# Kernel optimization log

Measured on AMD Instinct MI355X. Metric: run time of the kernel, lower is better.

The kernel has to match this reference:

```python
import jax, jax.numpy as jnp
import numpy as np


def conv2d(x, w, b):
    # x: [B,C,H,W], w: [O,I,5,5], VALID, stride 1 (matches torch Conv2d defaults)
    y = jax.lax.conv_general_dilated(x, w, (1, 1), 'VALID',
                                     dimension_numbers=('NCHW', 'OIHW', 'NCHW'))
    return y + b[None, :, None, None]


def maxpool_2x5(x):
    # MaxPool2d(kernel=(2,5), stride=(2,1))
    return jax.lax.reduce_window(x, -jnp.inf, jax.lax.max,
                                 (1, 1, 2, 5), (1, 1, 2, 1), 'VALID')


def gru(x, w_ih, w_hh, b_ih, b_hh):
    # Faithful torch nn.GRU (batch_first=False): x is [L, N, 64]; gate order r,z,n.
    H = w_hh.shape[1]
    h0 = jnp.zeros((x.shape[1], H), x.dtype)

    def step(h, xt):
        gi = xt @ w_ih.T + b_ih
        gh = h @ w_hh.T + b_hh
        i_r, i_z, i_n = jnp.split(gi, 3, axis=-1)
        h_r, h_z, h_n = jnp.split(gh, 3, axis=-1)
        r = jax.nn.sigmoid(i_r + h_r)
        z = jax.nn.sigmoid(i_z + h_z)
        n = jnp.tanh(i_n + r * h_n)
        h_new = (1.0 - z) * n + z * h
        return h_new, h_new

    _, ys = jax.lax.scan(step, h0, x)
    return ys


def branch(x, w1, b1, w2, b2, w3, b3, lw, lb, gwih, gwhh, gbih, gbhh):
    x = x[:, None]                      # [B,1,H,W]
    x = conv2d(x, w1, b1)
    x = conv2d(x, w2, b2)
    x = conv2d(x, w3, b3)
    x = maxpool_2x5(x)                  # [B,64,58,W']
    B = x.shape[0]
    x = x.reshape(B, x.shape[-1], 3712)  # same row-major reshape as torch
    x = x @ lw.T + lb                   # [B,W',64]
    # nn.GRU without batch_first scans over dim 0 (batch!) — replicate exactly
    return gru(x, gwih, gwhh, gbih, gbhh)


def _make_params(key):
    ks = iter(jax.random.split(key, 40))
    def p(shape, scale=0.05):
        return (jax.random.normal(next(ks), shape, jnp.float32) * scale)
    d = {}
    for pre in ('e', 't'):
        d[f'{pre}_w1'] = p((16, 1, 5, 5)); d[f'{pre}_b1'] = p((16,))
        d[f'{pre}_w2'] = p((32, 16, 5, 5)); d[f'{pre}_b2'] = p((32,))
        d[f'{pre}_w3'] = p((64, 32, 5, 5)); d[f'{pre}_b3'] = p((64,))
        d[f'{pre}l_w'] = p((64, 3712), 0.01); d[f'{pre}l_b'] = p((64,))
        d[f'{pre}g_wih'] = p((192, 64)); d[f'{pre}g_whh'] = p((192, 64))
        d[f'{pre}g_bih'] = p((192,)); d[f'{pre}g_bhh'] = p((192,))
    d['a_w'] = p((1, 64)); d['a_b'] = p((1,))
    d['h_w'] = p((128, 64)); d['h_b'] = p((128,))
    d['c_w'] = p((2, 128)); d['c_b'] = p((2,))
    return d


def setup_inputs() -> dict:
    key = jax.random.key(0)
    k1, k2, k3 = jax.random.split(key, 3)
    inp = {
        'evaluation': jax.random.normal(k1, (4, 128, 2048), jnp.float32),
        'template': jax.random.normal(k2, (4, 128, 1040), jnp.float32),
    }
    inp.update(_make_params(k3))
    return inp


def reference(evaluation, template,
              e_w1, e_b1, e_w2, e_b2, e_w3, e_b3, el_w, el_b,
              eg_wih, eg_whh, eg_bih, eg_bhh,
              t_w1, t_b1, t_w2, t_b2, t_w3, t_b3, tl_w, tl_b,
              tg_wih, tg_whh, tg_bih, tg_bhh,
              a_w, a_b, h_w, h_b, c_w, c_b):
    e = branch(evaluation, e_w1, e_b1, e_w2, e_b2, e_w3, e_b3,
               el_w, el_b, eg_wih, eg_whh, eg_bih, eg_bhh)   # [B,Se,64]
    t = branch(template, t_w1, t_b1, t_w2, t_b2, t_w3, t_b3,
               tl_w, tl_b, tg_wih, tg_whh, tg_bih, tg_bhh)   # [B,St,64]
    # bmm(template, eval^T) -> [B,St,Se], softmax over Se
    tt = jax.nn.softmax(jnp.einsum('btd,bed->bte', t, e), axis=-1)
    # bmm(tt^T, template) -> [B,Se,64]
    tt = jnp.einsum('bte,btd->bed', tt, t)
    tt = jnp.abs(tt - e)
    # attention over eval sequence positions
    att = jax.nn.softmax((e @ a_w.T + a_b)[..., 0], axis=-1)  # [B,Se]
    # vectorized form of the original Python double loop
    red = jnp.einsum('bed,be->bd', tt, att)                   # [B,64]
    h = jax.nn.relu(red @ h_w.T + h_b)
    return jax.nn.softmax(h @ c_w.T + c_b, axis=-1)           # [B,2]
```

## Files before the change

### kernel.cpp

```cpp
#include <hip/hip_runtime.h>
#include <cmath>


typedef unsigned short u16;
typedef unsigned int u32;
typedef __attribute__((ext_vector_type(8))) short bf16x8;
typedef __attribute__((ext_vector_type(8))) unsigned short u16x8;
typedef __attribute__((ext_vector_type(16))) float f32x16;

__device__ __forceinline__ u16 f2bf(float f) {
  unsigned int x = __float_as_uint(f);
  return (u16)((x + 0x7fffu + ((x >> 16) & 1u)) >> 16);
}
__device__ __forceinline__ float bf2f(u16 v) {
  return __uint_as_float(((unsigned int)v) << 16);
}

static const size_t OFF_BEFF_E  = 0;
static const size_t OFF_BEFF_T  = 64;
static const size_t OFF_BIAS2_E = 128;
static const size_t OFF_BIAS2_T = 320;
static const size_t OFF_WKX_E   = 512;
static const size_t OFF_WKX_T   = 27136;
static const size_t OFF_W12P_E  = 53760;
static const size_t OFF_W12P_T  = 63008;
static const size_t OFF_B12_E   = 72256;
static const size_t OFF_B12_T   = 72288;
static const size_t OFF_LWBF_E  = 72320;
static const size_t OFF_LWBF_T  = 191104;
static const size_t OFF_ATT     = 309888;
static const size_t OFF_XYBF_E  = 318016;
static const size_t OFF_XYBF_T  = 578112;
static const size_t OFF_TTBF    = 709184;
static const size_t OFF_LIN_E   = 840256;
static const size_t OFF_LIN_T   = 1360448;
static const size_t OFF_PV      = 1622592;
static const size_t OFF_RED     = 2142784;
static const size_t ZERO_F4     = 325696;
static const size_t OFF_POOL_E  = 2143040;
static const size_t OFF_POOL_T  = 17228608;
static const size_t OFF_GI_E    = 2143040;
static const size_t OFF_GI_T    = 3703616;
static const size_t OFF_P       = 4490048;

__global__ __launch_bounds__(320) void prep_kernel(
    const float* __restrict__ w1e, const float* __restrict__ b1e,
    const float* __restrict__ w2e, const float* __restrict__ b2e,
    const float* __restrict__ w1t, const float* __restrict__ b1t,
    const float* __restrict__ w2t, const float* __restrict__ b2t,
    float* __restrict__ w12p_e, float* __restrict__ w12p_t,
    float* __restrict__ b12o_e, float* __restrict__ b12o_t,
    const float* __restrict__ wih_e, const float* __restrict__ bih_e,
    const float* __restrict__ lb_e, float* __restrict__ bias2_e,
    const float* __restrict__ wih_t, const float* __restrict__ bih_t,
    const float* __restrict__ lb_t, float* __restrict__ bias2_t,
    const float* __restrict__ lwe, const float* __restrict__ lwt,
    u16* __restrict__ lwbf_e, u16* __restrict__ lwbf_t,
    float4* __restrict__ zbase) {
  const int bx = blockIdx.x;
  const int tid = threadIdx.x;
  {
    const size_t base = (size_t)bx * 615;
    const float4 z = {0.f, 0.f, 0.f, 0.f};
    for (size_t i = base + tid; i < base + 615 && i < ZERO_F4; i += 320)
      zbase[i] = z;
  }
  if (bx >= 66) {
    if (tid < 256) {
      const int k = bx - 66;
      const int br = k / 232, j = k - br * 232;
      const float* src = br ? lwt : lwe;
      u16* dst = br ? lwbf_t : lwbf_e;
      const int i = (j * 256 + tid) * 4;
      const float4 v = *(const float4*)&src[i];
      dst[i] = f2bf(v.x); dst[i + 1] = f2bf(v.y);
      dst[i + 2] = f2bf(v.z); dst[i + 3] = f2bf(v.w);
    }
    return;
  }
  if (bx >= 64) {
    const int br = bx - 64;
    const float* wih = br ? wih_t : wih_e;
    const float* bih = br ? bih_t : bih_e;
    const float* lb = br ? lb_t : lb_e;
    float* bias2 = br ? bias2_t : bias2_e;
    __shared__ float s_lb[64];
    if (tid < 64) s_lb[tid] = lb[tid];
    __syncthreads();
    if (tid < 192) {
      float acc = bih[tid];
      const float* wr = wih + tid * 64;
      for (int d = 0; d < 64; ++d) acc = fmaf(wr[d], s_lb[d], acc);
      bias2[tid] = acc;
    }
    return;
  }
  const int br = bx >> 5;
  const float* w1 = br ? w1t : w1e;
  const float* b1 = br ? b1t : b1e;
  const float* w2 = br ? w2t : w2e;
  const float* b2 = br ? b2t : b2e;
  float* w12p = br ? w12p_t : w12p_e;
  float* b12o = br ? b12o_t : b12o_e;
  const int c12 = bx & 31;
  __shared__ float s_w1pad[16 * 169];
  __shared__ float s_w2c[400];
  __shared__ float s_b1[16];
  for (int i = tid; i < 2704; i += 320) s_w1pad[i] = 0.f;
  if (tid < 16) s_b1[tid] = b1[tid];
  __syncthreads();
  for (int i = tid; i < 400; i += 320) {
    const int c1 = i / 25, r = (i % 25) / 5, cc = i % 5;
    s_w1pad[c1 * 169 + (r + 4) * 13 + (cc + 4)] = w1[i];
    s_w2c[i] = w2[c12 * 400 + i];
  }
  __syncthreads();
  if (tid < 289) {
    const int py = tid / 17, px = tid % 17;
    float v = 0.f;
    if (py >= 4 && py <= 12 && px >= 4 && px <= 12) {
      const int sy = py - 4, sx = px - 4;
      float accs[2] = {0.f, 0.f};
      for (int c1 = 0; c1 < 16; ++c1) {
        const float* w2p = s_w2c + c1 * 25;
        const float* w1p = s_w1pad + c1 * 169 + (sy + 4) * 13 + (sx + 4);
#pragma unroll
        for (int uy = 0; uy < 5; ++uy)
#pragma unroll
          for (int ux = 0; ux < 5; ++ux)
            accs[uy & 1] = fmaf(w2p[uy * 5 + ux], w1p[-(uy * 13) - ux], accs[uy & 1]);
      }
      v = accs[0] + accs[1];
    }
    w12p[c12 * 289 + tid] = v;
  } else if (tid == 300) {
    float acc = b2[c12];
    for (int c1 = 0; c1 < 16; ++c1) {
      float sw = 0.f;
      for (int u = 0; u < 25; ++u) sw += s_w2c[c1 * 25 + u];
      acc = fmaf(sw, s_b1[c1], acc);
    }
    b12o[c12] = acc;
  }
}

__global__ __launch_bounds__(256) void compose_weff_kernel(
    const float* __restrict__ w3e, const float* __restrict__ b3e,
    const float* __restrict__ w3t, const float* __restrict__ b3t,
    const float* __restrict__ w12p_e, const float* __restrict__ w12p_t,
    const float* __restrict__ b12_e, const float* __restrict__ b12_t,
    u16* __restrict__ wkx_e, u16* __restrict__ wkx_t,
    float* __restrict__ beff_e, float* __restrict__ beff_t) {
  const int br = blockIdx.y;
  const float* w3 = br ? w3t : w3e;
  const float* b3 = br ? b3t : b3e;
  const float* w12p = br ? w12p_t : w12p_e;
  const float* b12 = br ? b12_t : b12_e;
  u16* wkx = br ? wkx_t : wkx_e;
  float* beff = br ? beff_t : beff_e;
  const int o = blockIdx.x;
  __shared__ float s_pad[32 * 289];
  __shared__ float s_w3o[800];
  __shared__ float s_b12[32];
  const int tid = threadIdx.x;
  for (int i = tid; i < 9248; i += 256) s_pad[i] = w12p[i];
  for (int i = tid; i < 800; i += 256) s_w3o[i] = w3[o * 800 + i];
  if (tid < 32) s_b12[tid] = b12[tid];
  __syncthreads();
  if (tid < 169) {
    const int sy = tid / 13, sx = tid % 13;
    float accs[4] = {0.f, 0.f, 0.f, 0.f};
#pragma unroll 4
    for (int c = 0; c < 32; ++c) {
      const float* w3p = s_w3o + c * 25;
      const float* wp = s_pad + c * 289 + (sy + 4) * 17 + (sx + 4);
#pragma unroll
      for (int uy = 0; uy < 5; ++uy)
#pragma unroll
        for (int ux = 0; ux < 5; ++ux)
          accs[c & 3] = fmaf(w3p[uy * 5 + ux], wp[-(uy * 17) - ux], accs[c & 3]);
    }
    const u16 v = f2bf(accs[0] + accs[1] + accs[2] + accs[3]);
#pragma unroll
    for (int p = 0; p < 4; ++p)
      wkx[((p * 13 + sx) * 64 + o) * 16 + sy + p] = v;
  } else if (tid < 169 + 156) {
    const int t = tid - 169, kx = t / 12, q = t % 12;
    const int p = q / 3, idx = q % 3;
    const int slot = (idx < p) ? idx : (p + 13) + (idx - p);
    wkx[((p * 13 + kx) * 64 + o) * 16 + slot] = 0;
  } else if (tid == 330 - 5) {
  }
  if (tid == 255) {
    float acc = b3[o];
    for (int c = 0; c < 32; ++c) {
      float sw = 0.f;
      for (int u = 0; u < 25; ++u) sw += s_w3o[c * 25 + u];
      acc = fmaf(sw, s_b12[c], acc);
    }
    beff[o] = acc;
  }
}

__global__ __launch_bounds__(256, 4) void conv_pool_mfma_kernel(
    const float* __restrict__ xe, const u16* __restrict__ wkx_e,
    const float* __restrict__ beff_e, u16* __restrict__ pooled_e,
    const float* __restrict__ xt, const u16* __restrict__ wkx_t,
    const float* __restrict__ beff_t, u16* __restrict__ pooled_t) {
  const int zz = blockIdx.z;
  const bool ev = zz < 4;
  const int b = ev ? zz : zz - 4;
  const int W = ev ? 2048 : 1040;
  const int T = ev ? 2032 : 1024;
  const int cb = blockIdx.x * 60;
  if (cb >= T) return;
  const float* x = ev ? xe : xt;
  const u16* wkx = ev ? wkx_e : wkx_t;
  const float* beff = ev ? beff_e : beff_t;
  u16* pooled = ev ? pooled_e : pooled_t;

  __shared__ __align__(16) u16 s_x[80 * 24];
  __shared__ __align__(16) u16 s_out[2 * 64 * 66];
  __shared__ __align__(16) u16 s_pool[64 * 62];

  const int tid = threadIdx.x;
  const int lane = tid & 63, wave = tid >> 6;
  const int by = blockIdx.y;
  const int rsel = wave & 1, cm = (wave >> 1) * 32;
  const int l31 = lane & 31, g8 = (lane >> 5) * 8;
  const int r0 = 4 * by;

  {
    const float* xb = x + ((size_t)b * 128 + r0) * W;
    for (int i = tid; i < 640; i += 256) {
      const int pr = i / 80, c = i - pr * 80;
      int gc = cb + c;
      if (gc > W - 1) gc = W - 1;
      const u16 v0 = f2bf(xb[(size_t)(2 * pr) * W + gc]);
      const u16 v1 = f2bf(xb[(size_t)(2 * pr + 1) * W + gc]);
      *(u32*)&s_x[c * 24 + 2 * pr] = (u32)v0 | ((u32)v1 << 16);
    }
  }
  __syncthreads();
#pragma unroll
  for (int hh = 0; hh < 2; ++hh) {
    const int p = 2 * hh + rsel;
    const int h = 2 * by + hh;
    bf16x8 wfrag[13];
    {
      const u16* aw = wkx + ((p * 13) * 64 + cm + l31) * 16 + g8;
#pragma unroll
      for (int kx = 0; kx < 13; ++kx) wfrag[kx] = *(const bf16x8*)(aw + kx * 1024);
    }
    f32x16 acc0 = {}, acc1 = {};
    const u16* bx = s_x + g8;
#pragma unroll
    for (int kx = 0; kx < 13; ++kx) {
      bf16x8 b0 = *(const bf16x8*)(bx + (l31 + kx) * 24);
      bf16x8 b1 = *(const bf16x8*)(bx + (32 + l31 + kx) * 24);
      acc0 = __builtin_amdgcn_mfma_f32_32x32x16_bf16(wfrag[kx], b0, acc0, 0, 0, 0);
      acc1 = __builtin_amdgcn_mfma_f32_32x32x16_bf16(wfrag[kx], b1, acc1, 0, 0, 0);
    }
#pragma unroll
    for (int r = 0; r < 16; ++r) {
      const int c = cm + (r & 3) + 8 * (r >> 2) + (g8 >> 1);
      u16* o = s_out + (rsel * 64 + c) * 66;
      o[l31] = f2bf(acc0[r]);
      o[32 + l31] = f2bf(acc1[r]);
    }
    __syncthreads();
    {
      const int pc = tid & 63, tg = tid >> 6;
      const int t0 = tg * 15;
      const float bias = beff[pc];
      const u16* r0p = s_out + pc * 66 + t0;
      const u16* r1p = s_out + (64 + pc) * 66 + t0;
      float m01[19];
#pragma unroll
      for (int j = 0; j < 19; ++j) m01[j] = fmaxf(bf2f(r0p[j]), bf2f(r1p[j]));
#pragma unroll
      for (int i = 0; i < 15; ++i) {
        float m = m01[i];
#pragma unroll
        for (int k = 1; k < 5; ++k) m = fmaxf(m, m01[i + k]);
        s_pool[pc * 62 + t0 + i] = f2bf(m + bias);
      }
    }
    __syncthreads();
    for (int i = tid; i < 1920; i += 256) {
      const int c = i / 30, tp = i - c * 30;
      const int gt = cb + 2 * tp;
      if (gt < T) {
        const u32 pair = *(const u32*)&s_pool[c * 62 + 2 * tp];
        *(u32*)&pooled[(((size_t)b * 64 + c) * 58 + h) * T + gt] = pair;
      }
    }
  }
}

__global__ __launch_bounds__(256) void gemm_splitk_mfma_kernel(
    const u16* __restrict__ Ae, const u16* __restrict__ Bwe, float* __restrict__ oute,
    const u16* __restrict__ At, const u16* __restrict__ Bwt, float* __restrict__ outt) {
  const int bx = blockIdx.x;
  const bool ev = bx < 127;
  const u16* A = ev ? Ae : At;
  const u16* Bw = ev ? Bwe : Bwt;
  float* out = ev ? oute : outt;
  const int r0 = (ev ? bx : bx - 127) * 64;
  __shared__ __align__(16) u16 sA[64 * 72];
  __shared__ __align__(16) u16 sB[64 * 72];
  const int tid = threadIdx.x;
  const int s = blockIdx.y;
  const int ch0 = (s * 58) / 8, ch1 = ((s + 1) * 58) / 8;
  const int lane = tid & 63, wave = tid >> 6;
  const int l31 = lane & 31, g8 = (lane >> 5) * 8;
  const int mh = (wave & 1) * 32, nh = (wave >> 1) * 32;
  const int srow = tid >> 2, sseg = (tid & 3) * 16;
  f32x16 acc = {};
  for (int ch = ch0; ch < ch1; ++ch) {
    const int kc = ch * 64;
    __syncthreads();
    {
      const u16* ap = &A[(size_t)(r0 + srow) * 3712 + kc + sseg];
      const u16* bp = &Bw[(size_t)srow * 3712 + kc + sseg];
      u16* da = &sA[srow * 72 + sseg];
      u16* db = &sB[srow * 72 + sseg];
      *(u16x8*)da = *(const u16x8*)ap;
      *(u16x8*)(da + 8) = *(const u16x8*)(ap + 8);
      *(u16x8*)db = *(const u16x8*)bp;
      *(u16x8*)(db + 8) = *(const u16x8*)(bp + 8);
    }
    __syncthreads();
#pragma unroll
    for (int ks = 0; ks < 4; ++ks) {
      bf16x8 a = *(const bf16x8*)&sA[(mh + l31) * 72 + ks * 16 + g8];
      bf16x8 b = *(const bf16x8*)&sB[(nh + l31) * 72 + ks * 16 + g8];
      acc = __builtin_amdgcn_mfma_f32_32x32x16_bf16(a, b, acc, 0, 0, 0);
    }
  }
#pragma unroll
  for (int r = 0; r < 16; ++r) {
    const int row = mh + (r & 3) + 8 * (r >> 2) + (g8 >> 1);
    atomicAdd(&out[(size_t)(r0 + row) * 64 + nh + l31], acc[r]);
  }
}

__global__ __launch_bounds__(256) void gemm_gi_kernel(
    const float* __restrict__ Ae, const float* __restrict__ Wte,
    const float* __restrict__ biase, float* __restrict__ oute,
    const float* __restrict__ At, const float* __restrict__ Wtt,
    const float* __restrict__ biast, float* __restrict__ outt) {
  const int bx = blockIdx.x;
  const bool ev = bx < 127;
  const float* A = ev ? Ae : At;
  const float* Wt = ev ? Wte : Wtt;
  const float* bias = ev ? biase : biast;
  float* out = ev ? oute : outt;
  const int r0 = (ev ? bx : bx - 127) * 64;
  const int N = 192, K = 64;
  __shared__ float sA[64 * 33];
  __shared__ float sB[64 * 33];
  const int tid = threadIdx.x;
  const int n0 = blockIdx.y * 64;
  const int ty = tid >> 4, tx = tid & 15;
  float acc[4][4] = {};
  for (int kc = 0; kc < K; kc += 32) {
    __syncthreads();
#pragma unroll
    for (int rep = 0; rep < 8; ++rep) {
      const int l = tid + rep * 256;
      const int row = l >> 5, kk = l & 31;
      sA[row * 33 + kk] = A[(size_t)(r0 + row) * K + kc + kk];
      sB[row * 33 + kk] = Wt[(size_t)(n0 + row) * K + kc + kk];
    }
    __syncthreads();
#pragma unroll 8
    for (int kk = 0; kk < 32; ++kk) {
      const float a0 = sA[(ty * 4 + 0) * 33 + kk];
      const float a1 = sA[(ty * 4 + 1) * 33 + kk];
      const float a2 = sA[(ty * 4 + 2) * 33 + kk];
      const float a3 = sA[(ty * 4 + 3) * 33 + kk];
      const float b0 = sB[(tx * 4 + 0) * 33 + kk];
      const float b1 = sB[(tx * 4 + 1) * 33 + kk];
      const float b2 = sB[(tx * 4 + 2) * 33 + kk];
      const float b3 = sB[(tx * 4 + 3) * 33 + kk];
      acc[0][0] = fmaf(a0, b0, acc[0][0]); acc[0][1] = fmaf(a0, b1, acc[0][1]);
      acc[0][2] = fmaf(a0, b2, acc[0][2]); acc[0][3] = fmaf(a0, b3, acc[0][3]);
      acc[1][0] = fmaf(a1, b0, acc[1][0]); acc[1][1] = fmaf(a1, b1, acc[1][1]);
      acc[1][2] = fmaf(a1, b2, acc[1][2]); acc[1][3] = fmaf(a1, b3, acc[1][3]);
      acc[2][0] = fmaf(a2, b0, acc[2][0]); acc[2][1] = fmaf(a2, b1, acc[2][1]);
      acc[2][2] = fmaf(a2, b2, acc[2][2]); acc[2][3] = fmaf(a2, b3, acc[2][3]);
      acc[3][0] = fmaf(a3, b0, acc[3][0]); acc[3][1] = fmaf(a3, b1, acc[3][1]);
      acc[3][2] = fmaf(a3, b2, acc[3][2]); acc[3][3] = fmaf(a3, b3, acc[3][3]);
    }
  }
#pragma unroll
  for (int i = 0; i < 4; ++i)
#pragma unroll
    for (int j = 0; j < 4; ++j)
      out[(size_t)(r0 + ty * 4 + i) * N + n0 + tx * 4 + j] =
          acc[i][j] + bias[n0 + tx * 4 + j];
}

__global__ __launch_bounds__(256) void gru_rec_kernel(
    float* __restrict__ xyE, const float* __restrict__ giE,
    const float* __restrict__ whhE, const float* __restrict__ bhhE,
    float* __restrict__ xyT, const float* __restrict__ giT,
    const float* __restrict__ whhT, const float* __restrict__ bhhT,
    u16* __restrict__ xybfE, u16* __restrict__ xybfT, u16* __restrict__ ttbf,
    const float* __restrict__ a_w, const float* __restrict__ a_b,
    float* __restrict__ logits) {
  const int bxid = blockIdx.x;
  const bool ev = bxid < 127;
  float* xy = ev ? xyE : xyT;
  u16* xybf = ev ? xybfE : xybfT;
  const float* gi = ev ? giE : giT;
  const float* whh = ev ? whhE : whhT;
  const float* bhh = ev ? bhhE : bhhT;
  const int T = ev ? 2032 : 1024;
  const int t0 = (ev ? bxid : bxid - 127) * 16;
  __shared__ float s_whh_t[64 * 192];
  __shared__ float s_h[16][64];
  __shared__ float s_aw[64];
  const int tid = threadIdx.x;
  const int lane = tid & 63, wave = tid >> 6;
  for (int i = tid; i < 192 * 64; i += 256) {
    const int j = i >> 6, d = i & 63;
    s_whh_t[d * 192 + j] = whh[i];
  }
  for (int i = tid; i < 16 * 64; i += 256) (&s_h[0][0])[i] = 0.f;
  if (tid < 64) s_aw[tid] = a_w[tid];
  const float ab = a_b[0];
  const float bhr = bhh[lane], bhz = bhh[64 + lane], bhn = bhh[128 + lane];
  __syncthreads();
  for (int b = 0; b < 4; ++b) {
    float gir[4], giz[4], gin[4];
#pragma unroll
    for (int sl = 0; sl < 4; ++sl) {
      int t = t0 + wave * 4 + sl; if (t > T - 1) t = T - 1;
      const float* girow = gi + ((size_t)b * T + t) * 192;
      gir[sl] = girow[lane]; giz[sl] = girow[64 + lane]; gin[sl] = girow[128 + lane];
    }
    float ahr[4] = {}, ahz[4] = {}, ahn[4] = {};
    for (int d = 0; d < 64; ++d) {
      const float wr_ = s_whh_t[d * 192 + lane];
      const float wz_ = s_whh_t[d * 192 + 64 + lane];
      const float wn_ = s_whh_t[d * 192 + 128 + lane];
#pragma unroll
      for (int sl = 0; sl < 4; ++sl) {
        const float hv = s_h[wave * 4 + sl][d];
        ahr[sl] = fmaf(wr_, hv, ahr[sl]);
        ahz[sl] = fmaf(wz_, hv, ahz[sl]);
        ahn[sl] = fmaf(wn_, hv, ahn[sl]);
      }
    }
    float hn[4];
#pragma unroll
    for (int sl = 0; sl < 4; ++sl) {
      const float r = 1.f / (1.f + __expf(-(gir[sl] + ahr[sl] + bhr)));
      const float z = 1.f / (1.f + __expf(-(giz[sl] + ahz[sl] + bhz)));
      const float n = tanhf(gin[sl] + r * (ahn[sl] + bhn));
      hn[sl] = (1.f - z) * n + z * s_h[wave * 4 + sl][lane];
    }
    __syncthreads();
#pragma unroll
    for (int sl = 0; sl < 4; ++sl) {
      const int t = t0 + wave * 4 + sl;
      s_h[wave * 4 + sl][lane] = hn[sl];
      if (t < T) {
        const size_t idx = ((size_t)b * T + t) * 64 + lane;
        xy[idx] = hn[sl];
        xybf[idx] = f2bf(hn[sl]);
        if (ev) {
          float v = hn[sl] * s_aw[lane];
#pragma unroll
          for (int off = 32; off > 0; off >>= 1) v += __shfl_down(v, off, 64);
          if (lane == 0) logits[b * 2032 + t] = v + ab;
        } else {
          ttbf[((size_t)b * 64 + lane) * 1024 + t] = f2bf(hn[sl]);
        }
      }
    }
    __syncthreads();
  }
}

__global__ __launch_bounds__(256) void scores_mfma_kernel(
    const u16* __restrict__ tbf, const u16* __restrict__ ebf,
    u16* __restrict__ P) {
  __shared__ __align__(16) u16 sA[64 * 72];
  __shared__ __align__(16) u16 sB[128 * 72];
  const int tid = threadIdx.x;
  const int b = blockIdx.z;
  const int tau0 = blockIdx.x * 64;
  const int e0 = blockIdx.y * 128;
  const int lane = tid & 63, wave = tid >> 6;
  const int l31 = lane & 31, g8 = (lane >> 5) * 8;
  {
    const int row = tid >> 2, seg = (tid & 3) * 16;
    const u16* ap = &tbf[((size_t)b * 1024 + tau0 + row) * 64 + seg];
    u16* da = &sA[row * 72 + seg];
    *(u16x8*)da = *(const u16x8*)ap;
    *(u16x8*)(da + 8) = *(const u16x8*)(ap + 8);
  }
#pragma unroll
  for (int r = 0; r < 4; ++r) {
    const int q = tid + r * 256;
    const int row = q >> 3, seg = (q & 7) * 8;
    int eps = e0 + row; if (eps > 2031) eps = 2031;
    *(u16x8*)&sB[row * 72 + seg] =
        *(const u16x8*)&ebf[((size_t)b * 2032 + eps) * 64 + seg];
  }
  __syncthreads();
  const int mh = (wave & 1) * 32;
  const int nq = (wave >> 1) * 64;
  f32x16 acc0 = {}, acc1 = {};
#pragma unroll
  for (int ks = 0; ks < 4; ++ks) {
    bf16x8 a = *(const bf16x8*)&sA[(mh + l31) * 72 + ks * 16 + g8];
    bf16x8 b0 = *(const bf16x8*)&sB[(nq + l31) * 72 + ks * 16 + g8];
    bf16x8 b1 = *(const bf16x8*)&sB[(nq + 32 + l31) * 72 + ks * 16 + g8];
    acc0 = __builtin_amdgcn_mfma_f32_32x32x16_bf16(a, b0, acc0, 0, 0, 0);
    acc1 = __builtin_amdgcn_mfma_f32_32x32x16_bf16(a, b1, acc1, 0, 0, 0);
  }
#pragma unroll
  for (int r = 0; r < 16; ++r) {
    const int tau = tau0 + mh + (r & 3) + 8 * (r >> 2) + (g8 >> 1);
    const size_t prow = ((size_t)b * 1024 + tau) * 2032;
    const int ep0 = e0 + nq + l31;
    if (ep0 < 2032) P[prow + ep0] = f2bf(acc0[r]);
    const int ep1 = ep0 + 32;
    if (ep1 < 2032) P[prow + ep1] = f2bf(acc1[r]);
  }
}

__global__ __launch_bounds__(256) void softmax_rows_kernel(u16* __restrict__ P) {
  __shared__ float s_row[2032];
  __shared__ float sred[4];
  u16* r = P + (size_t)blockIdx.x * 2032;
  const int tid = threadIdx.x;
  const int lane = tid & 63, wave = tid >> 6;
  float m = -3.4e38f;
  for (int i = tid; i < 2032; i += 256) {
    const float v = bf2f(r[i]);
    s_row[i] = v;
    m = fmaxf(m, v);
  }
#pragma unroll
  for (int off = 32; off > 0; off >>= 1) m = fmaxf(m, __shfl_down(m, off, 64));
  if (lane == 0) sred[wave] = m;
  __syncthreads();
  m = fmaxf(fmaxf(sred[0], sred[1]), fmaxf(sred[2], sred[3]));
  __syncthreads();
  float s = 0.f;
  float vals[8];
  int cnt = 0;
  for (int i = tid; i < 2032; i += 256) {
    const float v = __expf(s_row[i] - m);
    vals[cnt++] = v;
    s += v;
  }
#pragma unroll
  for (int off = 32; off > 0; off >>= 1) s += __shfl_down(s, off, 64);
  if (lane == 0) sred[wave] = s;
  __syncthreads();
  const float inv = 1.f / (sred[0] + sred[1] + sred[2] + sred[3]);
  cnt = 0;
  for (int i = tid; i < 2032; i += 256) r[i] = f2bf(vals[cnt++] * inv);
}

__global__ __launch_bounds__(256) void pv_mfma_kernel(
    const u16* __restrict__ P, const u16* __restrict__ ttbf,
    float* __restrict__ PV) {
  __shared__ __align__(16) u16 sPT[64 * 72];
  __shared__ __align__(16) u16 sTT[64 * 72];
  const int tid = threadIdx.x;
  const int b = blockIdx.z;
  const int e0 = blockIdx.x * 64;
  const int tau_base = blockIdx.y * 256;
  const int lane = tid & 63, wave = tid >> 6;
  const int l31 = lane & 31, g8 = (lane >> 5) * 8;
  const int mh = (wave & 1) * 32, nh = (wave >> 1) * 32;
  f32x16 acc = {};
  for (int cc = 0; cc < 4; ++cc) {
    const int tc = tau_base + cc * 64;
    __syncthreads();
#pragma unroll
    for (int k = 0; k < 2; ++k) {
      const int q = tid + k * 256;
      const int row = q >> 3, seg = (q & 7) * 8;
      int er = e0 + seg;
      if (er > 2032 - 8) er = 2032 - 8;
      const u16x8 v = *(const u16x8*)&P[((size_t)b * 1024 + tc + row) * 2032 + er];
#pragma unroll
      for (int j = 0; j < 8; ++j) sPT[(seg + j) * 72 + row] = v[j];
    }
#pragma unroll
    for (int k = 0; k < 2; ++k) {
      const int q = tid + k * 256;
      const int row = q >> 3, seg = (q & 7) * 8;
      *(u16x8*)&sTT[row * 72 + seg] =
          *(const u16x8*)&ttbf[((size_t)b * 64 + row) * 1024 + tc + seg];
    }
    __syncthreads();
#pragma unroll
    for (int ks = 0; ks < 4; ++ks) {
      bf16x8 a = *(const bf16x8*)&sPT[(mh + l31) * 72 + ks * 16 + g8];
      bf16x8 bb = *(const bf16x8*)&sTT[(nh + l31) * 72 + ks * 16 + g8];
      acc = __builtin_amdgcn_mfma_f32_32x32x16_bf16(a, bb, acc, 0, 0, 0);
    }
  }
#pragma unroll
  for (int r = 0; r < 16; ++r) {
    const int eps = e0 + mh + (r & 3) + 8 * (r >> 2) + (g8 >> 1);
    if (eps < 2032)
      atomicAdd(&PV[((size_t)b * 2032 + eps) * 64 + nh + l31], acc[r]);
  }
}

__global__ __launch_bounds__(256) void red_reduce_kernel(
    const float* __restrict__ emat, const float* __restrict__ PV,
    const float* __restrict__ logits, float* __restrict__ red) {
  __shared__ float s_att[2032];
  __shared__ float sred[4];
  __shared__ float s_part[4][64];
  const int tid = threadIdx.x;
  const int lane = tid & 63, wave = tid >> 6;
  const int b = blockIdx.y;
  float m = -3.4e38f;
  for (int i = tid; i < 2032; i += 256) {
    const float v = logits[b * 2032 + i];
    s_att[i] = v;
    m = fmaxf(m, v);
  }
#pragma unroll
  for (int off = 32; off > 0; off >>= 1) m = fmaxf(m, __shfl_down(m, off, 64));
  if (lane == 0) sred[wave] = m;
  __syncthreads();
  m = fmaxf(fmaxf(sred[0], sred[1]), fmaxf(sred[2], sred[3]));
  __syncthreads();
  float ssum = 0.f;
  for (int i = tid; i < 2032; i += 256) {
    const float v = __expf(s_att[i] - m);
    s_att[i] = v;
    ssum += v;
  }
#pragma unroll
  for (int off = 32; off > 0; off >>= 1) ssum += __shfl_down(ssum, off, 64);
  if (lane == 0) sred[wave] = ssum;
  __syncthreads();
  const float inv = 1.f / (sred[0] + sred[1] + sred[2] + sred[3]);
  const int i0 = blockIdx.x * 127;
  float acc = 0.f;
  for (int i = i0 + wave; i < i0 + 127; i += 4) {
    const size_t idx = ((size_t)b * 2032 + i) * 64 + lane;
    acc = fmaf(fabsf(PV[idx] - emat[idx]), s_att[i], acc);
  }
  s_part[wave][lane] = acc;
  __syncthreads();
  if (tid < 64)
    atomicAdd(&red[b * 64 + tid],
              (s_part[0][tid] + s_part[1][tid] + s_part[2][tid] + s_part[3][tid]) * inv);
}

__global__ __launch_bounds__(128) void mlp_kernel(
    const float* __restrict__ red, const float* __restrict__ h_w,
    const float* __restrict__ h_b, const float* __restrict__ c_w,
    const float* __restrict__ c_b, float* __restrict__ out) {
  __shared__ float s_red[64];
  __shared__ float s_hv[128];
  const int tid = threadIdx.x;
  const int b = blockIdx.x;
  if (tid < 64) s_red[tid] = red[b * 64 + tid];
  __syncthreads();
  {
    float acc = h_b[tid];
    const float* hw = h_w + tid * 64;
    for (int d = 0; d < 64; ++d) acc = fmaf(s_red[d], hw[d], acc);
    s_hv[tid] = fmaxf(acc, 0.f);
  }
  __syncthreads();
  if (tid == 0) {
    float l0 = c_b[0], l1 = c_b[1];
    for (int j = 0; j < 128; ++j) {
      l0 = fmaf(s_hv[j], c_w[j], l0);
      l1 = fmaf(s_hv[j], c_w[128 + j], l1);
    }
    const float mm = fmaxf(l0, l1);
    const float e0 = __expf(l0 - mm), e1 = __expf(l1 - mm);
    const float invs = 1.f / (e0 + e1);
    out[b * 2 + 0] = e0 * invs;
    out[b * 2 + 1] = e1 * invs;
  }
}

extern "C" void kernel_launch(void* const* d_in, const int* in_sizes, int n_in,
                              void* d_out, int out_size, void* d_ws, size_t ws_size,
                              hipStream_t stream) {
  const float* evaluation = (const float*)d_in[0];
  const float* templ      = (const float*)d_in[1];
  const float* e_w1 = (const float*)d_in[2];
  const float* e_b1 = (const float*)d_in[3];
  const float* e_w2 = (const float*)d_in[4];
  const float* e_b2 = (const float*)d_in[5];
  const float* e_w3 = (const float*)d_in[6];
  const float* e_b3 = (const float*)d_in[7];
  const float* el_w = (const float*)d_in[8];
  const float* el_b = (const float*)d_in[9];
  const float* eg_wih = (const float*)d_in[10];
  const float* eg_whh = (const float*)d_in[11];
  const float* eg_bih = (const float*)d_in[12];
  const float* eg_bhh = (const float*)d_in[13];
  const float* t_w1 = (const float*)d_in[14];
  const float* t_b1 = (const float*)d_in[15];
  const float* t_w2 = (const float*)d_in[16];
  const float* t_b2 = (const float*)d_in[17];
  const float* t_w3 = (const float*)d_in[18];
  const float* t_b3 = (const float*)d_in[19];
  const float* tl_w = (const float*)d_in[20];
  const float* tl_b = (const float*)d_in[21];
  const float* tg_wih = (const float*)d_in[22];
  const float* tg_whh = (const float*)d_in[23];
  const float* tg_bih = (const float*)d_in[24];
  const float* tg_bhh = (const float*)d_in[25];
  const float* a_w = (const float*)d_in[26];
  const float* a_b = (const float*)d_in[27];
  const float* h_w = (const float*)d_in[28];
  const float* h_b = (const float*)d_in[29];
  const float* c_w = (const float*)d_in[30];
  const float* c_b = (const float*)d_in[31];

  float* ws = (float*)d_ws;
  float* beff_e  = ws + OFF_BEFF_E;
  float* beff_t  = ws + OFF_BEFF_T;
  float* bias2_e = ws + OFF_BIAS2_E;
  float* bias2_t = ws + OFF_BIAS2_T;
  u16*   wkx_e   = (u16*)(ws + OFF_WKX_E);
  u16*   wkx_t   = (u16*)(ws + OFF_WKX_T);
  float* w12p_e  = ws + OFF_W12P_E;
  float* w12p_t  = ws + OFF_W12P_T;
  float* b12_e   = ws + OFF_B12_E;
  float* b12_t   = ws + OFF_B12_T;
  u16*   lwbf_e  = (u16*)(ws + OFF_LWBF_E);
  u16*   lwbf_t  = (u16*)(ws + OFF_LWBF_T);
  float* attbuf  = ws + OFF_ATT;
  u16*   xybf_e  = (u16*)(ws + OFF_XYBF_E);
  u16*   xybf_t  = (u16*)(ws + OFF_XYBF_T);
  u16*   ttbf    = (u16*)(ws + OFF_TTBF);
  float* lin_e   = ws + OFF_LIN_E;
  float* lin_t   = ws + OFF_LIN_T;
  float* PVbuf   = ws + OFF_PV;
  float* redbuf  = ws + OFF_RED;
  u16*   pool_e  = (u16*)(ws + OFF_POOL_E);
  u16*   pool_t  = (u16*)(ws + OFF_POOL_T);
  float* gi_e    = ws + OFF_GI_E;
  float* gi_t    = ws + OFF_GI_T;
  u16*   Pbuf    = (u16*)(ws + OFF_P);

  prep_kernel<<<530, 320, 0, stream>>>(
      e_w1, e_b1, e_w2, e_b2, t_w1, t_b1, t_w2, t_b2, w12p_e, w12p_t, b12_e, b12_t,
      eg_wih, eg_bih, el_b, bias2_e, tg_wih, tg_bih, tl_b, bias2_t,
      el_w, tl_w, lwbf_e, lwbf_t, (float4*)lin_e);
  compose_weff_kernel<<<dim3(64, 2), 256, 0, stream>>>(
      e_w3, e_b3, t_w3, t_b3, w12p_e, w12p_t, b12_e, b12_t, wkx_e, wkx_t, beff_e, beff_t);

  conv_pool_mfma_kernel<<<dim3(34, 29, 8), 256, 0, stream>>>(
      evaluation, wkx_e, beff_e, pool_e, templ, wkx_t, beff_t, pool_t);
  gemm_splitk_mfma_kernel<<<dim3(191, 8), 256, 0, stream>>>(
      pool_e, lwbf_e, lin_e, pool_t, lwbf_t, lin_t);
  gemm_gi_kernel<<<dim3(191, 3), 256, 0, stream>>>(
      lin_e, eg_wih, bias2_e, gi_e, lin_t, tg_wih, bias2_t, gi_t);
  gru_rec_kernel<<<191, 256, 0, stream>>>(
      lin_e, gi_e, eg_whh, eg_bhh, lin_t, gi_t, tg_whh, tg_bhh,
      xybf_e, xybf_t, ttbf, a_w, a_b, attbuf);

  scores_mfma_kernel<<<dim3(16, 16, 4), 256, 0, stream>>>(xybf_t, xybf_e, Pbuf);
  softmax_rows_kernel<<<4096, 256, 0, stream>>>(Pbuf);
  pv_mfma_kernel<<<dim3(32, 4, 4), 256, 0, stream>>>(Pbuf, ttbf, PVbuf);

  red_reduce_kernel<<<dim3(16, 4), 256, 0, stream>>>(lin_e, PVbuf, attbuf, redbuf);
  mlp_kernel<<<4, 128, 0, stream>>>(redbuf, h_w, h_b, c_w, c_b, (float*)d_out);
}
```

Before: 335.7 us.

## Fuse softmax into scores and PV kernels via atomic row sums

Removes the separate softmax_rows kernel. The scores kernel now writes exp(score) to P and accumulates per-row sums through shuffle reductions and atomicAdd into a zeroed buffer. The PV kernel normalizes P by the reciprocal row sum while staging it into shared memory. Packed bf16 conversions are also used in several places. This cuts a full read and write pass over the P matrix and one launch. It drops max-subtraction, so large scores could overflow, and it adds atomic contention.

Result: faster. 320.8 us (-4.5%).

```diff
diff --git a/kernel.cpp b/kernel.cpp
--- a/kernel.cpp
+++ b/kernel.cpp
@@ -1,4 +1,5 @@
 #include <hip/hip_runtime.h>
+#include <hip/hip_bf16.h>
 #include <cmath>
 
 
@@ -14,6 +15,12 @@
 }
 __device__ __forceinline__ float bf2f(u16 v) {
   return __uint_as_float(((unsigned int)v) << 16);
+}
+__device__ __forceinline__ u32 f2bf_pk(float a, float b) {
+  __hip_bfloat162 h = __float22bfloat162_rn(float2{a, b});
+  u32 r;
+  __builtin_memcpy(&r, &h, 4);
+  return r;
 }
 
 static const size_t OFF_BEFF_E  = 0;
@@ -36,12 +43,14 @@
 static const size_t OFF_LIN_T   = 1360448;
 static const size_t OFF_PV      = 1622592;
 static const size_t OFF_RED     = 2142784;
-static const size_t ZERO_F4     = 325696;
-static const size_t OFF_POOL_E  = 2143040;
-static const size_t OFF_POOL_T  = 17228608;
-static const size_t OFF_GI_E    = 2143040;
-static const size_t OFF_GI_T    = 3703616;
-static const size_t OFF_P       = 4490048;
+static const size_t OFF_RSUM    = 2143040;
+static const size_t ZERO_F4     = 326720;
+static const size_t ZSTRIDE     = 617;
+static const size_t OFF_POOL_E  = 2147136;
+static const size_t OFF_POOL_T  = 17232704;
+static const size_t OFF_GI_E    = 2147136;
+static const size_t OFF_GI_T    = 3707712;
+static const size_t OFF_P       = 4494144;
 
 __global__ __launch_bounds__(320) void prep_kernel(
     const float* __restrict__ w1e, const float* __restrict__ b1e,
@@ -60,9 +69,9 @@
   const int bx = blockIdx.x;
   const int tid = threadIdx.x;
   {
-    const size_t base = (size_t)bx * 615;
+    const size_t base = (size_t)bx * ZSTRIDE;
     const float4 z = {0.f, 0.f, 0.f, 0.f};
-    for (size_t i = base + tid; i < base + 615 && i < ZERO_F4; i += 320)
+    for (size_t i = base + tid; i < base + ZSTRIDE && i < ZERO_F4; i += 320)
       zbase[i] = z;
   }
   if (bx >= 66) {
@@ -73,8 +82,8 @@
       u16* dst = br ? lwbf_t : lwbf_e;
       const int i = (j * 256 + tid) * 4;
       const float4 v = *(const float4*)&src[i];
-      dst[i] = f2bf(v.x); dst[i + 1] = f2bf(v.y);
-      dst[i + 2] = f2bf(v.z); dst[i + 3] = f2bf(v.w);
+      *(u32*)&dst[i] = f2bf_pk(v.x, v.y);
+      *(u32*)&dst[i + 2] = f2bf_pk(v.z, v.w);
     }
     return;
   }
@@ -189,7 +198,6 @@
     const int p = q / 3, idx = q % 3;
     const int slot = (idx < p) ? idx : (p + 13) + (idx - p);
     wkx[((p * 13 + kx) * 64 + o) * 16 + slot] = 0;
-  } else if (tid == 330 - 5) {
   }
   if (tid == 255) {
     float acc = b3[o];
@@ -236,9 +244,8 @@
       const int pr = i / 80, c = i - pr * 80;
       int gc = cb + c;
       if (gc > W - 1) gc = W - 1;
-      const u16 v0 = f2bf(xb[(size_t)(2 * pr) * W + gc]);
-      const u16 v1 = f2bf(xb[(size_t)(2 * pr + 1) * W + gc]);
-      *(u32*)&s_x[c * 24 + 2 * pr] = (u32)v0 | ((u32)v1 << 16);
+      *(u32*)&s_x[c * 24 + 2 * pr] =
+          f2bf_pk(xb[(size_t)(2 * pr) * W + gc], xb[(size_t)(2 * pr + 1) * W + gc]);
     }
   }
   __syncthreads();
@@ -265,8 +272,9 @@
     for (int r = 0; r < 16; ++r) {
       const int c = cm + (r & 3) + 8 * (r >> 2) + (g8 >> 1);
       u16* o = s_out + (rsel * 64 + c) * 66;
-      o[l31] = f2bf(acc0[r]);
-      o[32 + l31] = f2bf(acc1[r]);
+      const u32 pk = f2bf_pk(acc0[r], acc1[r]);
+      o[l31] = (u16)pk;
+      o[32 + l31] = (u16)(pk >> 16);
     }
     __syncthreads();
     {
@@ -278,13 +286,22 @@
       float m01[19];
 #pragma unroll
       for (int j = 0; j < 19; ++j) m01[j] = fmaxf(bf2f(r0p[j]), bf2f(r1p[j]));
+      float mm[15];
 #pragma unroll
       for (int i = 0; i < 15; ++i) {
         float m = m01[i];
 #pragma unroll
         for (int k = 1; k < 5; ++k) m = fmaxf(m, m01[i + k]);
-        s_pool[pc * 62 + t0 + i] = f2bf(m + bias);
+        mm[i] = m + bias;
       }
+      u16* sp = s_pool + pc * 62 + t0;
+#pragma unroll
+      for (int i = 0; i < 14; i += 2) {
+        const u32 pk = f2bf_pk(mm[i], mm[i + 1]);
+        sp[i] = (u16)pk;
+        sp[i + 1] = (u16)(pk >> 16);
+      }
+      sp[14] = f2bf(mm[14]);
     }
     __syncthreads();
     for (int i = tid; i < 1920; i += 256) {
@@ -487,7 +504,7 @@
 
 __global__ __launch_bounds__(256) void scores_mfma_kernel(
     const u16* __restrict__ tbf, const u16* __restrict__ ebf,
-    u16* __restrict__ P) {
+    u16* __restrict__ P, float* __restrict__ rowsum) {
   __shared__ __align__(16) u16 sA[64 * 72];
   __shared__ __align__(16) u16 sB[128 * 72];
   const int tid = threadIdx.x;
@@ -523,55 +540,26 @@
     acc0 = __builtin_amdgcn_mfma_f32_32x32x16_bf16(a, b0, acc0, 0, 0, 0);
     acc1 = __builtin_amdgcn_mfma_f32_32x32x16_bf16(a, b1, acc1, 0, 0, 0);
   }
+  const int ep0 = e0 + nq + l31;
+  const int ep1 = ep0 + 32;
 #pragma unroll
   for (int r = 0; r < 16; ++r) {
     const int tau = tau0 + mh + (r & 3) + 8 * (r >> 2) + (g8 >> 1);
     const size_t prow = ((size_t)b * 1024 + tau) * 2032;
-    const int ep0 = e0 + nq + l31;
-    if (ep0 < 2032) P[prow + ep0] = f2bf(acc0[r]);
-    const int ep1 = ep0 + 32;
-    if (ep1 < 2032) P[prow + ep1] = f2bf(acc1[r]);
-  }
-}
-
-__global__ __launch_bounds__(256) void softmax_rows_kernel(u16* __restrict__ P) {
-  __shared__ float s_row[2032];
-  __shared__ float sred[4];
-  u16* r = P + (size_t)blockIdx.x * 2032;
-  const int tid = threadIdx.x;
-  const int lane = tid & 63, wave = tid >> 6;
-  float m = -3.4e38f;
-  for (int i = tid; i < 2032; i += 256) {
-    const float v = bf2f(r[i]);
-    s_row[i] = v;
-    m = fmaxf(m, v);
-  }
-#pragma unroll
-  for (int off = 32; off > 0; off >>= 1) m = fmaxf(m, __shfl_down(m, off, 64));
-  if (lane == 0) sred[wave] = m;
-  __syncthreads();
-  m = fmaxf(fmaxf(sred[0], sred[1]), fmaxf(sred[2], sred[3]));
-  __syncthreads();
-  float s = 0.f;
-  float vals[8];
-  int cnt = 0;
-  for (int i = tid; i < 2032; i += 256) {
-    const float v = __expf(s_row[i] - m);
-    vals[cnt++] = v;
-    s += v;
-  }
-#pragma unroll
-  for (int off = 32; off > 0; off >>= 1) s += __shfl_down(s, off, 64);
-  if (lane == 0) sred[wave] = s;
-  __syncthreads();
-  const float inv = 1.f / (sred[0] + sred[1] + sred[2] + sred[3]);
-  cnt = 0;
-  for (int i = tid; i < 2032; i += 256) r[i] = f2bf(vals[cnt++] * inv);
+    const float e0v = __expf(acc0[r]);
+    const float e1v = __expf(acc1[r]);
+    float part = 0.f;
+    if (ep0 < 2032) { P[prow + ep0] = f2bf(e0v); part += e0v; }
+    if (ep1 < 2032) { P[prow + ep1] = f2bf(e1v); part += e1v; }
+#pragma unroll
+    for (int off = 16; off > 0; off >>= 1) part += __shfl_down(part, off, 32);
+    if (l31 == 0) atomicAdd(&rowsum[b * 1024 + tau], part);
+  }
 }
 
 __global__ __launch_bounds__(256) void pv_mfma_kernel(
     const u16* __restrict__ P, const u16* __restrict__ ttbf,
-    float* __restrict__ PV) {
+    const float* __restrict__ rowsum, float* __restrict__ PV) {
   __shared__ __align__(16) u16 sPT[64 * 72];
   __shared__ __align__(16) u16 sTT[64 * 72];
   const int tid = threadIdx.x;
@@ -589,11 +577,13 @@
     for (int k = 0; k < 2; ++k) {
       const int q = tid + k * 256;
       const int row = q >> 3, seg = (q & 7) * 8;
+      const float inv = 1.0f / rowsum[b * 1024 + tc + row];
       int er = e0 + seg;
       if (er > 2032 - 8) er = 2032 - 8;
       const u16x8 v = *(const u16x8*)&P[((size_t)b * 1024 + tc + row) * 2032 + er];
 #pragma unroll
-      for (int j = 0; j < 8; ++j) sPT[(seg + j) * 72 + row] = v[j];
+      for (int j = 0; j < 8; ++j)
+        sPT[(seg + j) * 72 + row] = f2bf(bf2f(v[j]) * inv);
     }
 #pragma unroll
     for (int k = 0; k < 2; ++k) {
@@ -751,6 +741,7 @@
   float* lin_t   = ws + OFF_LIN_T;
   float* PVbuf   = ws + OFF_PV;
   float* redbuf  = ws + OFF_RED;
+  float* rsum    = ws + OFF_RSUM;
   u16*   pool_e  = (u16*)(ws + OFF_POOL_E);
   u16*   pool_t  = (u16*)(ws + OFF_POOL_T);
   float* gi_e    = ws + OFF_GI_E;
@@ -774,9 +765,8 @@
       lin_e, gi_e, eg_whh, eg_bhh, lin_t, gi_t, tg_whh, tg_bhh,
       xybf_e, xybf_t, ttbf, a_w, a_b, attbuf);
 
-  scores_mfma_kernel<<<dim3(16, 16, 4), 256, 0, stream>>>(xybf_t, xybf_e, Pbuf);
-  softmax_rows_kernel<<<4096, 256, 0, stream>>>(Pbuf);
-  pv_mfma_kernel<<<dim3(32, 4, 4), 256, 0, stream>>>(Pbuf, ttbf, PVbuf);
+  scores_mfma_kernel<<<dim3(16, 16, 4), 256, 0, stream>>>(xybf_t, xybf_e, Pbuf, rsum);
+  pv_mfma_kernel<<<dim3(32, 4, 4), 256, 0, stream>>>(Pbuf, ttbf, rsum, PVbuf);
 
   red_reduce_kernel<<<dim3(16, 4), 256, 0, stream>>>(lin_e, PVbuf, attbuf, redbuf);
   mlp_kernel<<<4, 128, 0, stream>>>(redbuf, h_w, h_b, c_w, c_b, (float*)d_out);
```
